# Kernel optimization log

Measured on AMD Instinct MI355X. Metric: run time of the kernel, lower is better.

## Reference

```python
import jax, jax.numpy as jnp
import numpy as np

N_NODES = 100000
N_EDGES = 3200000
N_FEAT = 128
N_GRAPHS = 64


def setup_inputs() -> dict:
    key = jax.random.key(0)
    ks = jax.random.split(key, 8)
    x = jax.random.normal(ks[0], (N_NODES, N_FEAT), dtype=jnp.float32)
    edge_index = jax.random.randint(ks[1], (2, N_EDGES), 0, N_NODES, dtype=jnp.int64)
    batch = jnp.sort(jax.random.randint(ks[2], (N_NODES,), 0, N_GRAPHS, dtype=jnp.int64))
    # GCNConv weights (glorot-style scale) and biases
    W1 = jax.random.normal(ks[3], (N_FEAT, 32), dtype=jnp.float32) / np.sqrt(N_FEAT)
    b1 = jnp.zeros((32,), dtype=jnp.float32)
    W2 = jax.random.normal(ks[4], (32, 16), dtype=jnp.float32) / np.sqrt(32.0)
    b2 = jnp.zeros((16,), dtype=jnp.float32)
    lin_w = jax.random.normal(ks[5], (16, 1), dtype=jnp.float32) / np.sqrt(16.0)
    lin_b = jnp.zeros((1,), dtype=jnp.float32)
    return {"x": x, "edge_index": edge_index, "batch": batch,
            "W1": W1, "b1": b1, "W2": W2, "b2": b2,
            "lin_w": lin_w, "lin_b": lin_b}


def _gcn_conv(x, W, b, src, dst, deg_inv_sqrt, n_nodes):
    # transform first (fewer features downstream when out_dim < in_dim)
    xw = x @ W  # [N, out]
    norm = deg_inv_sqrt[src] * deg_inv_sqrt[dst]  # [E+N]
    msg = xw[src] * norm[:, None]  # gather + scale
    out = jax.ops.segment_sum(msg, dst, num_segments=n_nodes)  # scatter-add
    return out + b


def reference(x, edge_index, batch, W1, b1, W2, b2, lin_w, lin_b):
    n_nodes = x.shape[0]
    self_loop = jnp.arange(n_nodes, dtype=edge_index.dtype)
    src = jnp.concatenate([edge_index[0], self_loop])
    dst = jnp.concatenate([edge_index[1], self_loop])
    # symmetric GCN normalization with self-loops
    deg = jax.ops.segment_sum(jnp.ones_like(src, dtype=x.dtype), dst,
                              num_segments=n_nodes)
    deg_inv_sqrt = jnp.where(deg > 0, jax.lax.rsqrt(jnp.maximum(deg, 1.0)), 0.0)

    h = _gcn_conv(x, W1, b1, src, dst, deg_inv_sqrt, n_nodes)
    h = jax.nn.relu(h)
    # F.dropout with training=False (eval) is identity
    h = _gcn_conv(h, W2, b2, src, dst, deg_inv_sqrt, n_nodes)

    # global_mean_pool over batch index
    sums = jax.ops.segment_sum(h, batch, num_segments=N_GRAPHS)  # [G,16]
    cnts = jax.ops.segment_sum(jnp.ones((n_nodes,), dtype=h.dtype), batch,
                               num_segments=N_GRAPHS)
    pooled = sums / jnp.maximum(cnts, 1.0)[:, None]
    return pooled @ lin_w + lin_b  # [G,1]
```

## Files before the change

### kernel.cpp

```cpp
#include <hip/hip_runtime.h>

#define NN 100000
#define NE 3200000
#define NF 128
#define C1 32
#define C2 16
#define NG 64
#define BKT_SH 7
#define BKT_W  128
#define NBKT   782
#define CH     8192
#define NW     391
#define RSTR   784
#define MAPCAP 6400

#define OFF_BCNT  0
#define OFF_BST   1024
#define OFF_RUN   2048
#define OFF_ROW   308608
#define OFF_DIS   408624
#define OFF_POOL  508624
#define OFF_CNTF  509648
#define OFF_EDG   509712
#define OFF_XS1H0 OFF_EDG
#define OFF_XS1H1 (OFF_EDG + NN*8)
#define OFF_H1A   (OFF_EDG + NE)
#define OFF_XS2B  (OFF_H1A + NN*16)
#define OFF_COL   (OFF_XS2B + NN*8)

__device__ __forceinline__ unsigned pack_bf2(float a, float b) {
    unsigned ua = __float_as_uint(a);
    unsigned ub = __float_as_uint(b);
    ua = (ua + 0x7fffu + ((ua >> 16) & 1u)) >> 16;
    ub = (ub + 0x7fffu + ((ub >> 16) & 1u)) & 0xffff0000u;
    return ua | ub;
}
__device__ __forceinline__ float2 unpack_bf2(unsigned u) {
    return make_float2(__uint_as_float(u << 16), __uint_as_float(u & 0xffff0000u));
}
__device__ __forceinline__ void acc4(float4& a, uint2 q) {
    float2 f0 = unpack_bf2(q.x), f1 = unpack_bf2(q.y);
    a.x += f0.x; a.y += f0.y; a.z += f1.x; a.w += f1.y;
}

__global__ __launch_bounds__(256) void k_part(
    const int* __restrict__ S, const int* __restrict__ D,
    unsigned* __restrict__ edgebuf, int* __restrict__ runstart,
    int* __restrict__ bcnt)
{
    __shared__ int lhist[1024];
    __shared__ int lstart[1024];
    __shared__ int lcur[NBKT];
    __shared__ int sd[256];
    __shared__ unsigned lsort[CH];
    const int w = blockIdx.x;
    const int t = threadIdx.x;
    const int e0 = w * CH;
    const int n = min(CH, NE - e0);

    for (int i = t; i < 1024; i += 256) lhist[i] = 0;
    __syncthreads();
    for (int i = t; i < n; i += 256)
        atomicAdd(&lhist[(unsigned)D[e0 + i] >> BKT_SH], 1);
    __syncthreads();
    for (int i = t; i < NBKT; i += 256) atomicAdd(&bcnt[i], lhist[i]);
    int c0 = lhist[t * 4 + 0], c1 = lhist[t * 4 + 1];
    int c2 = lhist[t * 4 + 2], c3 = lhist[t * 4 + 3];
    int ts = c0 + c1 + c2 + c3;
    sd[t] = ts;
    __syncthreads();
    for (int off = 1; off < 256; off <<= 1) {
        int v = (t >= off) ? sd[t - off] : 0;
        __syncthreads();
        sd[t] += v;
        __syncthreads();
    }
    int excl = sd[t] - ts;
    lstart[t * 4 + 0] = excl;
    lstart[t * 4 + 1] = excl + c0;
    lstart[t * 4 + 2] = excl + c0 + c1;
    lstart[t * 4 + 3] = excl + c0 + c1 + c2;
    __syncthreads();
    for (int i = t; i < 783; i += 256) runstart[w * RSTR + i] = lstart[i];
    for (int i = t; i < NBKT; i += 256) lcur[i] = lstart[i];
    __syncthreads();
    for (int i = t; i < n; i += 256) {
        int s = S[e0 + i], d = D[e0 + i];
        int pos = atomicAdd(&lcur[(unsigned)d >> BKT_SH], 1);
        lsort[pos] = ((unsigned)s << BKT_SH) | (unsigned)(d & (BKT_W - 1));
    }
    __syncthreads();
    for (int i = t; i < n; i += 256) edgebuf[e0 + i] = lsort[i];
}

__global__ __launch_bounds__(256) void k_bscan(const int* __restrict__ bcnt,
                                               int* __restrict__ bstart,
                                               int* __restrict__ rowstart) {
    __shared__ int sd[256];
    const int t = threadIdx.x;
    const int base = t * 4;
    int c0 = (base + 0 < NBKT) ? bcnt[base + 0] : 0;
    int c1 = (base + 1 < NBKT) ? bcnt[base + 1] : 0;
    int c2 = (base + 2 < NBKT) ? bcnt[base + 2] : 0;
    int c3 = (base + 3 < NBKT) ? bcnt[base + 3] : 0;
    int ts = c0 + c1 + c2 + c3;
    sd[t] = ts;
    __syncthreads();
    for (int off = 1; off < 256; off <<= 1) {
        int v = (t >= off) ? sd[t - off] : 0;
        __syncthreads();
        sd[t] += v;
        __syncthreads();
    }
    int excl = sd[t] - ts;
    if (base + 0 < 783) bstart[base + 0] = excl;
    if (base + 1 < 783) bstart[base + 1] = excl + c0;
    if (base + 2 < 783) bstart[base + 2] = excl + c0 + c1;
    if (base + 3 < 783) bstart[base + 3] = excl + c0 + c1 + c2;
    if (t == 0) rowstart[NN] = NE;
}

__global__ __launch_bounds__(256) void k_fillfused(
    const unsigned* __restrict__ edgebuf, const int* __restrict__ runstart,
    const int* __restrict__ bstart,
    int* __restrict__ rowstart, float* __restrict__ dis, int* __restrict__ colidx)
{
    __shared__ int rl[NW];
    __shared__ int pfx[NW];
    __shared__ int basea[NW];
    __shared__ unsigned short map[MAPCAP];
    __shared__ int lcnt[BKT_W];
    __shared__ int lcur[BKT_W];
    __shared__ int sd[256];
    const int b = blockIdx.x;
    const int t = threadIdx.x;
    const int bs = bstart[b];
    const int total = bstart[b + 1] - bs;

    for (int w = t; w < NW; w += 256) {
        int s0 = runstart[w * RSTR + b];
        int s1 = runstart[w * RSTR + b + 1];
        basea[w] = s0;
        rl[w] = s1 - s0;
    }
    if (t < BKT_W) lcnt[t] = 0;
    __syncthreads();
    {
        int w0 = t * 2;
        int c0 = (w0 < NW) ? rl[w0] : 0;
        int c1 = (w0 + 1 < NW) ? rl[w0 + 1] : 0;
        int ts = c0 + c1;
        sd[t] = ts;
        __syncthreads();
        for (int off = 1; off < 256; off <<= 1) {
            int v = (t >= off) ? sd[t - off] : 0;
            __syncthreads();
            sd[t] += v;
            __syncthreads();
        }
        int excl = sd[t] - ts;
        if (w0 < NW)     pfx[w0]     = excl;
        if (w0 + 1 < NW) pfx[w0 + 1] = excl + c0;
    }
    __syncthreads();
    for (int w = t; w < NW; w += 256) {
        int p = pfx[w], len = rl[w];
        basea[w] = w * CH + basea[w] - p;
        for (int i = 0; i < len; ++i) map[p + i] = (unsigned short)w;
    }
    __syncthreads();
    for (int j = t; j < total; j += 256) {
        unsigned p = edgebuf[basea[map[j]] + j];
        atomicAdd(&lcnt[p & (BKT_W - 1)], 1);
    }
    __syncthreads();
    if (t < BKT_W) lcur[t] = lcnt[t];
    __syncthreads();
    for (int off = 1; off < BKT_W; off <<= 1) {
        int v = (t < BKT_W && t >= off) ? lcur[t - off] : 0;
        __syncthreads();
        if (t < BKT_W) lcur[t] += v;
        __syncthreads();
    }
    if (t < BKT_W) {
        int excl = lcur[t] - lcnt[t];
        int node = b * BKT_W + t;
        if (node < NN) {
            rowstart[node] = bs + excl;
            dis[node] = rsqrtf((float)lcnt[t] + 1.0f);
        }
        lcur[t] = bs + excl;
    }
    __syncthreads();
    for (int j = t; j < total; j += 256) {
        unsigned p = edgebuf[basea[map[j]] + j];
        int pos = atomicAdd(&lcur[p & (BKT_W - 1)], 1);
        colidx[pos] = (int)(p >> BKT_SH);
    }
}

__global__ __launch_bounds__(256) void k_gemm1(
    const float* __restrict__ x, const float* __restrict__ W1,
    const float* __restrict__ dis,
    unsigned* __restrict__ xs1h0, unsigned* __restrict__ xs1h1)
{
    __shared__ float xls[128 * 33];
    __shared__ float wls[32 * 32];
    const int t = threadIdx.x;
    const int tc = t & 7;
    const int tr = t >> 3;
    const int base = blockIdx.x * 128;

    float a[4][4] = {};

    for (int k0 = 0; k0 < NF; k0 += 32) {
        {
            int i = t * 4;
            int kk = i >> 5, c = i & 31;
            *(float4*)&wls[kk * 32 + c] = *(const float4*)&W1[(k0 + kk) * C1 + c];
        }
        #pragma unroll
        for (int r = 0; r < 4; ++r) {
            int n = (t >> 3) + r * 32;
            int j = (t & 7) * 4;
            int node = base + n;
            float4 v = make_float4(0.f, 0.f, 0.f, 0.f);
            if (node < NN) v = *(const float4*)&x[(long long)node * NF + k0 + j];
            xls[n * 33 + j + 0] = v.x;
            xls[n * 33 + j + 1] = v.y;
            xls[n * 33 + j + 2] = v.z;
            xls[n * 33 + j + 3] = v.w;
        }
        __syncthreads();
        #pragma unroll 8
        for (int kk = 0; kk < 32; ++kk) {
            float4 w = *(const float4*)&wls[kk * 32 + tc * 4];
            #pragma unroll
            for (int i = 0; i < 4; ++i) {
                float xv = xls[(tr * 4 + i) * 33 + kk];
                a[i][0] = fmaf(xv, w.x, a[i][0]);
                a[i][1] = fmaf(xv, w.y, a[i][1]);
                a[i][2] = fmaf(xv, w.z, a[i][2]);
                a[i][3] = fmaf(xv, w.w, a[i][3]);
            }
        }
        __syncthreads();
    }
    #pragma unroll
    for (int i = 0; i < 4; ++i) {
        int node = base + tr * 4 + i;
        if (node < NN) {
            float dv = dis[node];
            uint2 o;
            o.x = pack_bf2(a[i][0] * dv, a[i][1] * dv);
            o.y = pack_bf2(a[i][2] * dv, a[i][3] * dv);
            unsigned* dst = (tc < 4) ? &xs1h0[node * 8 + tc * 2]
                                     : &xs1h1[node * 8 + (tc - 4) * 2];
            *(uint2*)dst = o;
        }
    }
}

template<int HALF>
__global__ __launch_bounds__(256) void k_gather1h(
    const unsigned* __restrict__ xsh, const int* __restrict__ colidx,
    const int* __restrict__ rowstart, const float* __restrict__ dis,
    const float* __restrict__ b1, float* __restrict__ h1a,
    const float* __restrict__ W2, unsigned* __restrict__ xs2b)
{
    __shared__ float w2s[C1 * C2];
    __shared__ float hrow[64 * 33];
    const int t = threadIdx.x;
    if (HALF == 1 && t < 128) *(float4*)&w2s[t * 4] = *(const float4*)&W2[t * 4];
    const int l = t & 3;
    const int n = t >> 2;
    const int v = blockIdx.x * 64 + n;
    const bool valid = v < NN;

    float4 acc = make_float4(0.f, 0.f, 0.f, 0.f);
    float dv = 0.f;
    if (valid) {
        const int start = rowstart[v];
        const int num = rowstart[v + 1] - start;
        const int* __restrict__ cp = &colidx[start];
        uint2 u = *(const uint2*)&xsh[v * 8 + l * 2];
        float4 a0 = make_float4(0.f, 0.f, 0.f, 0.f);
        acc4(a0, u);
        float4 a1 = make_float4(0.f, 0.f, 0.f, 0.f), a2 = a1, a3 = a1;
        int i = 0;
        for (; i + 8 <= num; i += 8) {
            int s0 = cp[i], s1 = cp[i+1], s2 = cp[i+2], s3 = cp[i+3];
            int s4 = cp[i+4], s5 = cp[i+5], s6 = cp[i+6], s7 = cp[i+7];
            uint2 q0 = *(const uint2*)&xsh[s0 * 8 + l * 2];
            uint2 q1 = *(const uint2*)&xsh[s1 * 8 + l * 2];
            uint2 q2 = *(const uint2*)&xsh[s2 * 8 + l * 2];
            uint2 q3 = *(const uint2*)&xsh[s3 * 8 + l * 2];
            uint2 q4 = *(const uint2*)&xsh[s4 * 8 + l * 2];
            uint2 q5 = *(const uint2*)&xsh[s5 * 8 + l * 2];
            uint2 q6 = *(const uint2*)&xsh[s6 * 8 + l * 2];
            uint2 q7 = *(const uint2*)&xsh[s7 * 8 + l * 2];
            acc4(a0, q0); acc4(a1, q1); acc4(a2, q2); acc4(a3, q3);
            acc4(a0, q4); acc4(a1, q5); acc4(a2, q6); acc4(a3, q7);
        }
        for (; i < num; ++i) {
            uint2 q = *(const uint2*)&xsh[cp[i] * 8 + l * 2];
            acc4(a0, q);
        }
        acc.x = (a0.x + a1.x) + (a2.x + a3.x);
        acc.y = (a0.y + a1.y) + (a2.y + a3.y);
        acc.z = (a0.z + a1.z) + (a2.z + a3.z);
        acc.w = (a0.w + a1.w) + (a2.w + a3.w);
        dv = dis[v];
    }

    if (HALF == 0) {
        if (valid) {
            float4 o;
            o.x = fmaxf(fmaf(acc.x, dv, b1[l * 4 + 0]), 0.f);
            o.y = fmaxf(fmaf(acc.y, dv, b1[l * 4 + 1]), 0.f);
            o.z = fmaxf(fmaf(acc.z, dv, b1[l * 4 + 2]), 0.f);
            o.w = fmaxf(fmaf(acc.w, dv, b1[l * 4 + 3]), 0.f);
            *(float4*)&h1a[v * 16 + l * 4] = o;
        }
    } else {
        if (valid) {
            float4 hh = *(const float4*)&h1a[v * 16 + l * 4];
            hrow[n * 33 + l * 4 + 0] = hh.x;
            hrow[n * 33 + l * 4 + 1] = hh.y;
            hrow[n * 33 + l * 4 + 2] = hh.z;
            hrow[n * 33 + l * 4 + 3] = hh.w;
            hrow[n * 33 + 16 + l * 4 + 0] = fmaxf(fmaf(acc.x, dv, b1[16 + l * 4 + 0]), 0.f);
            hrow[n * 33 + 16 + l * 4 + 1] = fmaxf(fmaf(acc.y, dv, b1[16 + l * 4 + 1]), 0.f);
            hrow[n * 33 + 16 + l * 4 + 2] = fmaxf(fmaf(acc.z, dv, b1[16 + l * 4 + 2]), 0.f);
            hrow[n * 33 + 16 + l * 4 + 3] = fmaxf(fmaf(acc.w, dv, b1[16 + l * 4 + 3]), 0.f);
        }
        __syncthreads();
        if (valid) {
            const float* hr = &hrow[n * 33];
            float s0 = 0.f, s1 = 0.f, s2 = 0.f, s3 = 0.f;
            #pragma unroll
            for (int k = 0; k < 32; ++k) {
                float hv = hr[k];
                s0 = fmaf(hv, w2s[k * C2 + l * 4 + 0], s0);
                s1 = fmaf(hv, w2s[k * C2 + l * 4 + 1], s1);
                s2 = fmaf(hv, w2s[k * C2 + l * 4 + 2], s2);
                s3 = fmaf(hv, w2s[k * C2 + l * 4 + 3], s3);
            }
            uint2 o;
            o.x = pack_bf2(s0 * dv, s1 * dv);
            o.y = pack_bf2(s2 * dv, s3 * dv);
            *(uint2*)&xs2b[v * 8 + l * 2] = o;
        }
    }
}

__global__ __launch_bounds__(256) void k_gather2(
    const unsigned* __restrict__ xs2b, const int* __restrict__ colidx,
    const int* __restrict__ rowstart, const float* __restrict__ dis,
    const int* __restrict__ batch,
    float* __restrict__ pool, float* __restrict__ cntf)
{
    __shared__ float psum[NG * C2];
    __shared__ float cs[NG];
    const int t = threadIdx.x;
    for (int i = t; i < NG * C2; i += 256) psum[i] = 0.f;
    if (t < NG) cs[t] = 0.f;
    __syncthreads();

    const int l = t & 3;
    const int n = t >> 2;
    const int v = blockIdx.x * 64 + n;
    if (v < NN) {
        const int start = rowstart[v];
        const int num = rowstart[v + 1] - start;
        const int* __restrict__ cp = &colidx[start];
        uint2 u = *(const uint2*)&xs2b[v * 8 + l * 2];
        float4 a0 = make_float4(0.f, 0.f, 0.f, 0.f);
        acc4(a0, u);
        float4 a1 = make_float4(0.f, 0.f, 0.f, 0.f), a2 = a1, a3 = a1;
        int i = 0;
        for (; i + 8 <= num; i += 8) {
            int s0 = cp[i], s1 = cp[i+1], s2 = cp[i+2], s3 = cp[i+3];
            int s4 = cp[i+4], s5 = cp[i+5], s6 = cp[i+6], s7 = cp[i+7];
            uint2 q0 = *(const uint2*)&xs2b[s0 * 8 + l * 2];
            uint2 q1 = *(const uint2*)&xs2b[s1 * 8 + l * 2];
            uint2 q2 = *(const uint2*)&xs2b[s2 * 8 + l * 2];
            uint2 q3 = *(const uint2*)&xs2b[s3 * 8 + l * 2];
            uint2 q4 = *(const uint2*)&xs2b[s4 * 8 + l * 2];
            uint2 q5 = *(const uint2*)&xs2b[s5 * 8 + l * 2];
            uint2 q6 = *(const uint2*)&xs2b[s6 * 8 + l * 2];
            uint2 q7 = *(const uint2*)&xs2b[s7 * 8 + l * 2];
            acc4(a0, q0); acc4(a1, q1); acc4(a2, q2); acc4(a3, q3);
            acc4(a0, q4); acc4(a1, q5); acc4(a2, q6); acc4(a3, q7);
        }
        for (; i < num; ++i) {
            uint2 q = *(const uint2*)&xs2b[cp[i] * 8 + l * 2];
            acc4(a0, q);
        }
        float ax = (a0.x + a1.x) + (a2.x + a3.x);
        float ay = (a0.y + a1.y) + (a2.y + a3.y);
        float az = (a0.z + a1.z) + (a2.z + a3.z);
        float aw = (a0.w + a1.w) + (a2.w + a3.w);
        float dv = dis[v];
        int g = batch[v];
        atomicAdd(&psum[g * C2 + l * 4 + 0], ax * dv);
        atomicAdd(&psum[g * C2 + l * 4 + 1], ay * dv);
        atomicAdd(&psum[g * C2 + l * 4 + 2], az * dv);
        atomicAdd(&psum[g * C2 + l * 4 + 3], aw * dv);
        if (l == 0) atomicAdd(&cs[g], 1.0f);
    }
    __syncthreads();
    for (int i = t; i < NG * C2; i += 256)
        if (psum[i] != 0.f) atomicAdd(&pool[i], psum[i]);
    if (t < NG && cs[t] != 0.f) atomicAdd(&cntf[t], cs[t]);
}

__global__ void k_final(const float* __restrict__ pool, const float* __restrict__ cntf,
                        const float* __restrict__ b2,
                        const float* __restrict__ lw, const float* __restrict__ lb,
                        float* __restrict__ out)
{
    int g = threadIdx.x;
    if (g < NG) {
        float c = fmaxf(cntf[g], 1.0f);
        float inv = 1.0f / c;
        float s = lb[0];
        #pragma unroll
        for (int k = 0; k < C2; ++k) {
            s = fmaf(b2[k], lw[k], s);
            s = fmaf(pool[g * C2 + k] * inv, lw[k], s);
        }
        out[g] = s;
    }
}

extern "C" void kernel_launch(void* const* d_in, const int* in_sizes, int n_in,
                              void* d_out, int out_size, void* d_ws, size_t ws_size,
                              hipStream_t stream) {
    const float* x     = (const float*)d_in[0];
    const int*   ei    = (const int*)d_in[1];
    const int*   batch = (const int*)d_in[2];
    const float* W1    = (const float*)d_in[3];
    const float* b1    = (const float*)d_in[4];
    const float* W2    = (const float*)d_in[5];
    const float* b2    = (const float*)d_in[6];
    const float* lw    = (const float*)d_in[7];
    const float* lb    = (const float*)d_in[8];
    float* out = (float*)d_out;

    float*    wsf = (float*)d_ws;
    int*      wsi = (int*)d_ws;
    unsigned* wsu = (unsigned*)d_ws;

    int*      bcnt     = wsi + OFF_BCNT;
    int*      bstart   = wsi + OFF_BST;
    int*      runstart = wsi + OFF_RUN;
    int*      rowstart = wsi + OFF_ROW;
    float*    dis      = wsf + OFF_DIS;
    float*    pool     = wsf + OFF_POOL;
    float*    cntf     = wsf + OFF_CNTF;
    unsigned* edgebuf  = wsu + OFF_EDG;
    unsigned* xs1h0    = wsu + OFF_XS1H0;
    unsigned* xs1h1    = wsu + OFF_XS1H1;
    float*    h1a      = wsf + OFF_H1A;
    unsigned* xs2b     = wsu + OFF_XS2B;
    int*      colidx   = wsi + OFF_COL;

    const int* S = ei;
    const int* D = ei + NE;

    hipMemsetAsync(bcnt, 0, 1024 * sizeof(int), stream);
    hipMemsetAsync(pool, 0, (NG * C2 + NG) * sizeof(float), stream);

    k_part       <<<NW, 256, 0, stream>>>(S, D, edgebuf, runstart, bcnt);
    k_bscan      <<<1, 256, 0, stream>>>(bcnt, bstart, rowstart);
    k_fillfused  <<<NBKT, 256, 0, stream>>>(edgebuf, runstart, bstart, rowstart, dis, colidx);
    k_gemm1      <<<(NN + 127) / 128, 256, 0, stream>>>(x, W1, dis, xs1h0, xs1h1);
    k_gather1h<0><<<(NN + 63) / 64, 256, 0, stream>>>(xs1h0, colidx, rowstart, dis, b1, h1a, W2, xs2b);
    k_gather1h<1><<<(NN + 63) / 64, 256, 0, stream>>>(xs1h1, colidx, rowstart, dis, b1, h1a, W2, xs2b);
    k_gather2    <<<(NN + 63) / 64, 256, 0, stream>>>(xs2b, colidx, rowstart, dis, batch, pool, cntf);
    k_final      <<<1, 64, 0, stream>>>(pool, cntf, b2, lw, lb, out);
}
```

Measured before the change: 285.4 us.

## Merge split-half layer-1 gather into one full-width pass; widen partition block

```diff
diff --git a/kernel.cpp b/kernel.cpp
--- a/kernel.cpp
+++ b/kernel.cpp
@@ -22,10 +22,8 @@
 #define OFF_POOL  508624
 #define OFF_CNTF  509648
 #define OFF_EDG   509712
-#define OFF_XS1H0 OFF_EDG
-#define OFF_XS1H1 (OFF_EDG + NN*8)
-#define OFF_H1A   (OFF_EDG + NE)
-#define OFF_XS2B  (OFF_H1A + NN*16)
+#define OFF_XS1   OFF_EDG
+#define OFF_XS2B  (OFF_EDG + NE)
 #define OFF_COL   (OFF_XS2B + NN*8)
 
 __device__ __forceinline__ unsigned pack_bf2(float a, float b) {
@@ -43,7 +41,7 @@
     a.x += f0.x; a.y += f0.y; a.z += f1.x; a.w += f1.y;
 }
 
-__global__ __launch_bounds__(256) void k_part(
+__global__ __launch_bounds__(512) void k_part(
     const int* __restrict__ S, const int* __restrict__ D,
     unsigned* __restrict__ edgebuf, int* __restrict__ runstart,
     int* __restrict__ bcnt)
@@ -51,46 +49,49 @@
     __shared__ int lhist[1024];
     __shared__ int lstart[1024];
     __shared__ int lcur[NBKT];
-    __shared__ int sd[256];
+    __shared__ int wsum[8];
     __shared__ unsigned lsort[CH];
     const int w = blockIdx.x;
     const int t = threadIdx.x;
     const int e0 = w * CH;
     const int n = min(CH, NE - e0);
 
-    for (int i = t; i < 1024; i += 256) lhist[i] = 0;
-    __syncthreads();
-    for (int i = t; i < n; i += 256)
+    for (int i = t; i < 1024; i += 512) lhist[i] = 0;
+    __syncthreads();
+    for (int i = t; i < n; i += 512)
         atomicAdd(&lhist[(unsigned)D[e0 + i] >> BKT_SH], 1);
     __syncthreads();
-    for (int i = t; i < NBKT; i += 256) atomicAdd(&bcnt[i], lhist[i]);
-    int c0 = lhist[t * 4 + 0], c1 = lhist[t * 4 + 1];
-    int c2 = lhist[t * 4 + 2], c3 = lhist[t * 4 + 3];
-    int ts = c0 + c1 + c2 + c3;
-    sd[t] = ts;
-    __syncthreads();
-    for (int off = 1; off < 256; off <<= 1) {
-        int v = (t >= off) ? sd[t - off] : 0;
-        __syncthreads();
-        sd[t] += v;
-        __syncthreads();
-    }
-    int excl = sd[t] - ts;
-    lstart[t * 4 + 0] = excl;
-    lstart[t * 4 + 1] = excl + c0;
-    lstart[t * 4 + 2] = excl + c0 + c1;
-    lstart[t * 4 + 3] = excl + c0 + c1 + c2;
-    __syncthreads();
-    for (int i = t; i < 783; i += 256) runstart[w * RSTR + i] = lstart[i];
-    for (int i = t; i < NBKT; i += 256) lcur[i] = lstart[i];
-    __syncthreads();
-    for (int i = t; i < n; i += 256) {
+    for (int i = t; i < NBKT; i += 512) atomicAdd(&bcnt[i], lhist[i]);
+
+    int c0 = lhist[t * 2 + 0], c1 = lhist[t * 2 + 1];
+    int ts = c0 + c1;
+    const int lane = t & 63, wv = t >> 6;
+    int sc = ts;
+    #pragma unroll
+    for (int off = 1; off < 64; off <<= 1) {
+        int v = __shfl_up(sc, off, 64);
+        if (lane >= off) sc += v;
+    }
+    if (lane == 63) wsum[wv] = sc;
+    __syncthreads();
+    int wo = 0;
+    #pragma unroll
+    for (int i = 0; i < 8; ++i) wo += (i < wv) ? wsum[i] : 0;
+    int excl = sc - ts + wo;
+    lstart[t * 2 + 0] = excl;
+    lstart[t * 2 + 1] = excl + c0;
+    __syncthreads();
+
+    for (int i = t; i < 783; i += 512) runstart[w * RSTR + i] = lstart[i];
+    for (int i = t; i < NBKT; i += 512) lcur[i] = lstart[i];
+    __syncthreads();
+    for (int i = t; i < n; i += 512) {
         int s = S[e0 + i], d = D[e0 + i];
         int pos = atomicAdd(&lcur[(unsigned)d >> BKT_SH], 1);
         lsort[pos] = ((unsigned)s << BKT_SH) | (unsigned)(d & (BKT_W - 1));
     }
     __syncthreads();
-    for (int i = t; i < n; i += 256) edgebuf[e0 + i] = lsort[i];
+    for (int i = t; i < n; i += 512) edgebuf[e0 + i] = lsort[i];
 }
 
 __global__ __launch_bounds__(256) void k_bscan(const int* __restrict__ bcnt,
@@ -202,7 +203,7 @@
 __global__ __launch_bounds__(256) void k_gemm1(
     const float* __restrict__ x, const float* __restrict__ W1,
     const float* __restrict__ dis,
-    unsigned* __restrict__ xs1h0, unsigned* __restrict__ xs1h1)
+    unsigned* __restrict__ xs1)
 {
     __shared__ float xls[128 * 33];
     __shared__ float wls[32 * 32];
@@ -254,104 +255,72 @@
             uint2 o;
             o.x = pack_bf2(a[i][0] * dv, a[i][1] * dv);
             o.y = pack_bf2(a[i][2] * dv, a[i][3] * dv);
-            unsigned* dst = (tc < 4) ? &xs1h0[node * 8 + tc * 2]
-                                     : &xs1h1[node * 8 + (tc - 4) * 2];
-            *(uint2*)dst = o;
-        }
-    }
-}
-
-template<int HALF>
-__global__ __launch_bounds__(256) void k_gather1h(
-    const unsigned* __restrict__ xsh, const int* __restrict__ colidx,
+            *(uint2*)&xs1[node * 16 + tc * 2] = o;
+        }
+    }
+}
+
+__global__ __launch_bounds__(256) void k_gather1(
+    const unsigned* __restrict__ xs1, const int* __restrict__ colidx,
     const int* __restrict__ rowstart, const float* __restrict__ dis,
-    const float* __restrict__ b1, float* __restrict__ h1a,
-    const float* __restrict__ W2, unsigned* __restrict__ xs2b)
+    const float* __restrict__ b1, const float* __restrict__ W2,
+    unsigned* __restrict__ xs2b)
 {
     __shared__ float w2s[C1 * C2];
-    __shared__ float hrow[64 * 33];
-    const int t = threadIdx.x;
-    if (HALF == 1 && t < 128) *(float4*)&w2s[t * 4] = *(const float4*)&W2[t * 4];
-    const int l = t & 3;
-    const int n = t >> 2;
-    const int v = blockIdx.x * 64 + n;
-    const bool valid = v < NN;
-
-    float4 acc = make_float4(0.f, 0.f, 0.f, 0.f);
-    float dv = 0.f;
-    if (valid) {
-        const int start = rowstart[v];
-        const int num = rowstart[v + 1] - start;
-        const int* __restrict__ cp = &colidx[start];
-        uint2 u = *(const uint2*)&xsh[v * 8 + l * 2];
-        float4 a0 = make_float4(0.f, 0.f, 0.f, 0.f);
-        acc4(a0, u);
-        float4 a1 = make_float4(0.f, 0.f, 0.f, 0.f), a2 = a1, a3 = a1;
-        int i = 0;
-        for (; i + 8 <= num; i += 8) {
-            int s0 = cp[i], s1 = cp[i+1], s2 = cp[i+2], s3 = cp[i+3];
-            int s4 = cp[i+4], s5 = cp[i+5], s6 = cp[i+6], s7 = cp[i+7];
-            uint2 q0 = *(const uint2*)&xsh[s0 * 8 + l * 2];
-            uint2 q1 = *(const uint2*)&xsh[s1 * 8 + l * 2];
-            uint2 q2 = *(const uint2*)&xsh[s2 * 8 + l * 2];
-            uint2 q3 = *(const uint2*)&xsh[s3 * 8 + l * 2];
-            uint2 q4 = *(const uint2*)&xsh[s4 * 8 + l * 2];
-            uint2 q5 = *(const uint2*)&xsh[s5 * 8 + l * 2];
-            uint2 q6 = *(const uint2*)&xsh[s6 * 8 + l * 2];
-            uint2 q7 = *(const uint2*)&xsh[s7 * 8 + l * 2];
-            acc4(a0, q0); acc4(a1, q1); acc4(a2, q2); acc4(a3, q3);
-            acc4(a0, q4); acc4(a1, q5); acc4(a2, q6); acc4(a3, q7);
-        }
-        for (; i < num; ++i) {
-            uint2 q = *(const uint2*)&xsh[cp[i] * 8 + l * 2];
-            acc4(a0, q);
-        }
-        acc.x = (a0.x + a1.x) + (a2.x + a3.x);
-        acc.y = (a0.y + a1.y) + (a2.y + a3.y);
-        acc.z = (a0.z + a1.z) + (a2.z + a3.z);
-        acc.w = (a0.w + a1.w) + (a2.w + a3.w);
-        dv = dis[v];
-    }
-
-    if (HALF == 0) {
-        if (valid) {
-            float4 o;
-            o.x = fmaxf(fmaf(acc.x, dv, b1[l * 4 + 0]), 0.f);
-            o.y = fmaxf(fmaf(acc.y, dv, b1[l * 4 + 1]), 0.f);
-            o.z = fmaxf(fmaf(acc.z, dv, b1[l * 4 + 2]), 0.f);
-            o.w = fmaxf(fmaf(acc.w, dv, b1[l * 4 + 3]), 0.f);
-            *(float4*)&h1a[v * 16 + l * 4] = o;
-        }
-    } else {
-        if (valid) {
-            float4 hh = *(const float4*)&h1a[v * 16 + l * 4];
-            hrow[n * 33 + l * 4 + 0] = hh.x;
-            hrow[n * 33 + l * 4 + 1] = hh.y;
-            hrow[n * 33 + l * 4 + 2] = hh.z;
-            hrow[n * 33 + l * 4 + 3] = hh.w;
-            hrow[n * 33 + 16 + l * 4 + 0] = fmaxf(fmaf(acc.x, dv, b1[16 + l * 4 + 0]), 0.f);
-            hrow[n * 33 + 16 + l * 4 + 1] = fmaxf(fmaf(acc.y, dv, b1[16 + l * 4 + 1]), 0.f);
-            hrow[n * 33 + 16 + l * 4 + 2] = fmaxf(fmaf(acc.z, dv, b1[16 + l * 4 + 2]), 0.f);
-            hrow[n * 33 + 16 + l * 4 + 3] = fmaxf(fmaf(acc.w, dv, b1[16 + l * 4 + 3]), 0.f);
-        }
-        __syncthreads();
-        if (valid) {
-            const float* hr = &hrow[n * 33];
-            float s0 = 0.f, s1 = 0.f, s2 = 0.f, s3 = 0.f;
-            #pragma unroll
-            for (int k = 0; k < 32; ++k) {
-                float hv = hr[k];
-                s0 = fmaf(hv, w2s[k * C2 + l * 4 + 0], s0);
-                s1 = fmaf(hv, w2s[k * C2 + l * 4 + 1], s1);
-                s2 = fmaf(hv, w2s[k * C2 + l * 4 + 2], s2);
-                s3 = fmaf(hv, w2s[k * C2 + l * 4 + 3], s3);
-            }
-            uint2 o;
-            o.x = pack_bf2(s0 * dv, s1 * dv);
-            o.y = pack_bf2(s2 * dv, s3 * dv);
-            *(uint2*)&xs2b[v * 8 + l * 2] = o;
-        }
-    }
+    __shared__ float hrow[32 * 33];
+    const int t = threadIdx.x;
+    if (t < 128) *(float4*)&w2s[t * 4] = *(const float4*)&W2[t * 4];
+    const int l = t & 7;
+    const int n = t >> 3;
+    const int v = blockIdx.x * 32 + n;
+
+    const int start = rowstart[v];
+    const int num = rowstart[v + 1] - start;
+    const int* __restrict__ cp = &colidx[start];
+    uint2 u = *(const uint2*)&xs1[v * 16 + l * 2];
+    float4 a0 = make_float4(0.f, 0.f, 0.f, 0.f);
+    acc4(a0, u);
+    float4 a1 = make_float4(0.f, 0.f, 0.f, 0.f), a2 = a1, a3 = a1;
+    int i = 0;
+    for (; i + 8 <= num; i += 8) {
+        int s0 = cp[i], s1 = cp[i+1], s2 = cp[i+2], s3 = cp[i+3];
+        int s4 = cp[i+4], s5 = cp[i+5], s6 = cp[i+6], s7 = cp[i+7];
+        uint2 q0 = *(const uint2*)&xs1[s0 * 16 + l * 2];
+        uint2 q1 = *(const uint2*)&xs1[s1 * 16 + l * 2];
+        uint2 q2 = *(const uint2*)&xs1[s2 * 16 + l * 2];
+        uint2 q3 = *(const uint2*)&xs1[s3 * 16 + l * 2];
+        uint2 q4 = *(const uint2*)&xs1[s4 * 16 + l * 2];
+        uint2 q5 = *(const uint2*)&xs1[s5 * 16 + l * 2];
+        uint2 q6 = *(const uint2*)&xs1[s6 * 16 + l * 2];
+        uint2 q7 = *(const uint2*)&xs1[s7 * 16 + l * 2];
+        acc4(a0, q0); acc4(a1, q1); acc4(a2, q2); acc4(a3, q3);
+        acc4(a0, q4); acc4(a1, q5); acc4(a2, q6); acc4(a3, q7);
+    }
+    for (; i < num; ++i) {
+        uint2 q = *(const uint2*)&xs1[cp[i] * 16 + l * 2];
+        acc4(a0, q);
+    }
+    float ax = (a0.x + a1.x) + (a2.x + a3.x);
+    float ay = (a0.y + a1.y) + (a2.y + a3.y);
+    float az = (a0.z + a1.z) + (a2.z + a3.z);
+    float aw = (a0.w + a1.w) + (a2.w + a3.w);
+    const float dv = dis[v];
+
+    hrow[n * 33 + l * 4 + 0] = fmaxf(fmaf(ax, dv, b1[l * 4 + 0]), 0.f);
+    hrow[n * 33 + l * 4 + 1] = fmaxf(fmaf(ay, dv, b1[l * 4 + 1]), 0.f);
+    hrow[n * 33 + l * 4 + 2] = fmaxf(fmaf(az, dv, b1[l * 4 + 2]), 0.f);
+    hrow[n * 33 + l * 4 + 3] = fmaxf(fmaf(aw, dv, b1[l * 4 + 3]), 0.f);
+    __syncthreads();
+
+    const float* hr = &hrow[n * 33];
+    float s0 = 0.f, s1 = 0.f;
+    #pragma unroll
+    for (int k = 0; k < 32; ++k) {
+        float hv = hr[k];
+        s0 = fmaf(hv, w2s[k * C2 + 2 * l + 0], s0);
+        s1 = fmaf(hv, w2s[k * C2 + 2 * l + 1], s1);
+    }
+    xs2b[v * 8 + l] = pack_bf2(s0 * dv, s1 * dv);
 }
 
 __global__ __launch_bounds__(256) void k_gather2(
@@ -460,9 +429,7 @@
     float*    pool     = wsf + OFF_POOL;
     float*    cntf     = wsf + OFF_CNTF;
     unsigned* edgebuf  = wsu + OFF_EDG;
-    unsigned* xs1h0    = wsu + OFF_XS1H0;
-    unsigned* xs1h1    = wsu + OFF_XS1H1;
-    float*    h1a      = wsf + OFF_H1A;
+    unsigned* xs1      = wsu + OFF_XS1;
     unsigned* xs2b     = wsu + OFF_XS2B;
     int*      colidx   = wsi + OFF_COL;
 
@@ -472,12 +439,11 @@
     hipMemsetAsync(bcnt, 0, 1024 * sizeof(int), stream);
     hipMemsetAsync(pool, 0, (NG * C2 + NG) * sizeof(float), stream);
 
-    k_part       <<<NW, 256, 0, stream>>>(S, D, edgebuf, runstart, bcnt);
+    k_part       <<<NW, 512, 0, stream>>>(S, D, edgebuf, runstart, bcnt);
     k_bscan      <<<1, 256, 0, stream>>>(bcnt, bstart, rowstart);
     k_fillfused  <<<NBKT, 256, 0, stream>>>(edgebuf, runstart, bstart, rowstart, dis, colidx);
-    k_gemm1      <<<(NN + 127) / 128, 256, 0, stream>>>(x, W1, dis, xs1h0, xs1h1);
-    k_gather1h<0><<<(NN + 63) / 64, 256, 0, stream>>>(xs1h0, colidx, rowstart, dis, b1, h1a, W2, xs2b);
-    k_gather1h<1><<<(NN + 63) / 64, 256, 0, stream>>>(xs1h1, colidx, rowstart, dis, b1, h1a, W2, xs2b);
+    k_gemm1      <<<(NN + 127) / 128, 256, 0, stream>>>(x, W1, dis, xs1);
+    k_gather1    <<<NN / 32, 256, 0, stream>>>(xs1, colidx, rowstart, dis, b1, W2, xs2b);
     k_gather2    <<<(NN + 63) / 64, 256, 0, stream>>>(xs2b, colidx, rowstart, dis, batch, pool, cntf);
     k_final      <<<1, 64, 0, stream>>>(pool, cntf, b2, lw, lb, out);
 }
```

Measured after the change: 257.2 us. -9.9%, faster.
